# Optimization experiments

Measured on AMD Instinct MI355X. Metric: run time of the kernel, lower is better.

Reference implementation:

```python
import jax, jax.numpy as jnp
import numpy as np

B, T, D = 2, 2048, 1024
N, K, H = 16, 8, 128  # q heads, kv heads, head_dim
G = N // K            # GQA group size
EPS = 1e-6
THETA = 1000000.0
SCALE = H ** -0.5
K_MASK = float(np.finfo(np.float32).min)


def rms_norm(x, scale):
    # RMSNorm over head_dim (last axis), computed in fp32 like the original
    dtype = x.dtype
    rms = jnp.sqrt(jnp.mean(x.astype(jnp.float32) ** 2, axis=-1, keepdims=True) + EPS)
    return (scale * x / rms).astype(dtype)


def positions_from_segment_ids(seg):
    t = jnp.arange(seg.shape[1], dtype=jnp.int32)[None, :]
    off = jnp.argmax(seg, axis=1, keepdims=True).astype(jnp.int32)
    rel = t - off
    return jnp.where(seg != 0, rel, jnp.int32(2 ** 30))


def rope_sin_cos(positions):
    frac = jnp.arange(0, H, 2, dtype=jnp.float32) / H
    inv_freq = 1.0 / (THETA ** frac)                    # [H/2]
    ang = positions.astype(jnp.float32)[..., None] * inv_freq  # [B,T,H/2]
    return jnp.sin(ang), jnp.cos(ang)


def apply_rope(x, sin, cos):
    # x: [B,T,heads,H]; sin/cos: [B,T,H/2]
    x1, x2 = x[..., : H // 2], x[..., H // 2:]
    s, c = sin[:, :, None, :], cos[:, :, None, :]
    return jnp.concatenate([x1 * c - x2 * s, x2 * c + x1 * s], axis=-1).astype(x.dtype)


def setup_inputs() -> dict:
    key = jax.random.key(0)
    ks = jax.random.split(key, 8)
    std = 0.02
    return {
        "x": jax.random.normal(ks[0], (B, T, D), dtype=jnp.float32),
        "segment_ids": jnp.ones((B, T), dtype=jnp.int32),
        "wq": jax.random.normal(ks[1], (D, N, H), dtype=jnp.float32) * std,
        "wk": jax.random.normal(ks[2], (D, K, H), dtype=jnp.float32) * std,
        "wv": jax.random.normal(ks[3], (D, K, H), dtype=jnp.float32) * std,
        "wo": jax.random.normal(ks[4], (N, H, D), dtype=jnp.float32) * std,
        "q_scale": jnp.ones((H,), dtype=jnp.float32),
        "k_scale": jnp.ones((H,), dtype=jnp.float32),
    }


def reference(x, segment_ids, wq, wk, wv, wo, q_scale, k_scale):
    # QKV projections + QK RMSNorm
    q = rms_norm(jnp.einsum('BTD,DNH->BTNH', x, wq), q_scale)  # [B,T,N,H]
    k = rms_norm(jnp.einsum('BSD,DKH->BSKH', x, wk), k_scale)  # [B,T,K,H]
    v = jnp.einsum('BSD,DKH->BSKH', x, wv)                     # [B,T,K,H]

    # RoPE using segment-relative positions
    pos = positions_from_segment_ids(segment_ids)  # [B,T] int32
    sin, cos = rope_sin_cos(pos)
    q = apply_rope(q, sin, cos)
    k = apply_rope(k, sin, cos)

    # GQA attention: [B,T,K,G,H] x [B,S,K,H] -> [B,T,S,K,G]
    qg = q.reshape(B, T, K, G, H)
    logits = jnp.einsum('BTKGH,BSKH->BTSKG', qg, k) * SCALE

    causal = pos[:, None, :] <= pos[:, :, None]                       # [B,T,S]
    segm = segment_ids[:, None, :] == segment_ids[:, :, None]         # [B,T,S]
    mask = (causal & segm)[:, :, :, None, None]
    logits = jnp.where(mask, logits, K_MASK)

    w = jax.nn.softmax(logits.astype(jnp.float32), axis=2).astype(logits.dtype)
    out = jnp.einsum('BTSKG,BSKH->BTKGH', w, v).reshape(B, T, N, H)
    return jnp.einsum('BTNH,NHD->BTD', out, wo)
```

## Files before the change

### kernel.cpp

```cpp
#include <hip/hip_runtime.h>
#include <hip/hip_bf16.h>


typedef unsigned short u16;
typedef __attribute__((ext_vector_type(8))) short s16x8;
typedef __attribute__((ext_vector_type(4))) float fp32x4;
typedef __attribute__((ext_vector_type(4))) u16 u16x4;

#define MFMA_BF16(a, b, c) __builtin_amdgcn_mfma_f32_16x16x32_bf16((a), (b), (c), 0, 0, 0)

static constexpr int Bq = 2, Tq = 2048, Dq = 1024, NHq = 16, KHq = 8, Hq = 128;
static constexpr float EPSq = 1e-6f;
static constexpr float S2q = 0.08838834764831845f * 1.4426950408889634f;
static constexpr float MAXq = 20.0f;
static constexpr float NEGHUGE = -3.0e38f;

__device__ __forceinline__ u16 f2b(float f) {
  __hip_bfloat16 h = __float2bfloat16(f);
  return *reinterpret_cast<u16*>(&h);
}

__device__ __forceinline__ void gload16(const u16* g, u16* lds_base) {
  __builtin_amdgcn_global_load_lds(
      (const __attribute__((address_space(1))) unsigned int*)(const void*)g,
      (__attribute__((address_space(3))) unsigned int*)(void*)lds_base, 16, 0, 0);
}


__global__ __launch_bounds__(256) void prep_kernel(
    const float* __restrict__ x, const float* __restrict__ wq,
    const float* __restrict__ wk, const float* __restrict__ wv,
    const float* __restrict__ wo, const int* __restrict__ seg,
    u16* __restrict__ xb, u16* __restrict__ wqkv_t, u16* __restrict__ wo_t,
    int* __restrict__ pos) {
  const int bid = blockIdx.x;
  const int tid = threadIdx.x;
  if (bid < 4096) {
    const int i = bid * 1024 + tid * 4;
    const float4 v = *reinterpret_cast<const float4*>(x + i);
    u16x4 o;
    o.x = f2b(v.x); o.y = f2b(v.y); o.z = f2b(v.z); o.w = f2b(v.w);
    *reinterpret_cast<u16x4*>(xb + i) = o;
    return;
  }
  __shared__ float tile[32][33];
  __shared__ int sv[256], si[256];
  const int tx = tid & 31, ty = tid >> 5;
  if (bid < 8192) {
    const int z = bid - 4096;
    const int r0 = (z & 31) * 32;
    const int c0 = (z >> 5) * 32;
    const float* src;
    int stride, coff;
    if (c0 < 2048)      { src = wq; stride = 2048; coff = c0; }
    else if (c0 < 3072) { src = wk; stride = 1024; coff = c0 - 2048; }
    else                { src = wv; stride = 1024; coff = c0 - 3072; }
#pragma unroll
    for (int j = 0; j < 32; j += 8)
      tile[ty + j][tx] = src[(long)(r0 + ty + j) * stride + (coff + tx)];
    __syncthreads();
#pragma unroll
    for (int j = 0; j < 32; j += 8)
      wqkv_t[(long)(c0 + ty + j) * 1024 + (r0 + tx)] = f2b(tile[tx][ty + j]);
    return;
  }
  if (bid < 10240) {
    const int z = bid - 8192;
    const int c0 = (z & 31) * 32;
    const int r0 = (z >> 5) * 32;
#pragma unroll
    for (int j = 0; j < 32; j += 8)
      tile[ty + j][tx] = wo[(long)(r0 + ty + j) * 1024 + (c0 + tx)];
    __syncthreads();
#pragma unroll
    for (int j = 0; j < 32; j += 8)
      wo_t[(long)(c0 + ty + j) * 2048 + (r0 + tx)] = f2b(tile[tx][ty + j]);
    return;
  }
  const int b = bid - 10240;
  const int* s = seg + b * Tq;
  int bestv = -2147483647 - 1, besti = 0x7fffffff;
  for (int t = tid; t < Tq; t += 256) {
    int v = s[t];
    if (v > bestv) { bestv = v; besti = t; }
  }
  sv[tid] = bestv; si[tid] = besti;
  __syncthreads();
  for (int k = 128; k > 0; k >>= 1) {
    if (tid < k) {
      int v2 = sv[tid + k], i2 = si[tid + k];
      if (v2 > sv[tid] || (v2 == sv[tid] && i2 < si[tid])) {
        sv[tid] = v2; si[tid] = i2;
      }
    }
    __syncthreads();
  }
  const int off = si[0];
  for (int t = tid; t < Tq; t += 256)
    pos[b * Tq + t] = (s[t] != 0) ? (t - off) : (1 << 30);
}


__global__ __launch_bounds__(256) void gemm_qkv_kernel(
    const u16* __restrict__ A, const u16* __restrict__ Bt,
    u16* __restrict__ qkv, u16* __restrict__ vt, const int* __restrict__ pos,
    const float* __restrict__ q_scale, const float* __restrict__ k_scale) {
  __shared__ __align__(16) u16 As[128][64];
  __shared__ __align__(16) u16 Bs[128][64];
  const int tid = threadIdx.x;
  const int wave = tid >> 6, lane = tid & 63;
  const int quad = lane >> 4, l16 = lane & 15;
  const int m0 = blockIdx.y * 128, n0 = blockIdx.x * 128;
  const int row8 = lane >> 3;
  const int cgl = (lane & 7) ^ row8;

  const fp32x4 z4 = {0.f, 0.f, 0.f, 0.f};
  fp32x4 acc[2][8];
#pragma unroll
  for (int i = 0; i < 2; ++i)
#pragma unroll
    for (int j = 0; j < 8; ++j) acc[i][j] = z4;

  for (int k0 = 0; k0 < 1024; k0 += 64) {
    __syncthreads();
#pragma unroll
    for (int jj = 0; jj < 4; ++jj) {
      const int R = wave * 32 + jj * 8;
      gload16(A + (size_t)(m0 + R + row8) * 1024 + k0 + cgl * 8, &As[R][0]);
      gload16(Bt + (size_t)(n0 + R + row8) * 1024 + k0 + cgl * 8, &Bs[R][0]);
    }
    __syncthreads();
#pragma unroll
    for (int kh = 0; kh < 2; ++kh) {
      s16x8 af[2], bfr[8];
#pragma unroll
      for (int i = 0; i < 2; ++i)
        af[i] = *(const s16x8*)&As[wave * 32 + i * 16 + l16]
                               [((((kh << 2) | quad) ^ (l16 & 7)) << 3)];
#pragma unroll
      for (int j = 0; j < 8; ++j)
        bfr[j] = *(const s16x8*)&Bs[j * 16 + l16]
                                [((((kh << 2) | quad) ^ (l16 & 7)) << 3)];
#pragma unroll
      for (int i = 0; i < 2; ++i)
#pragma unroll
        for (int j = 0; j < 8; ++j) acc[i][j] = MFMA_BF16(af[i], bfr[j], acc[i][j]);
    }
  }

  const int wrow = m0 + wave * 32;
  if (n0 >= 3072) {
    const int kv8 = (n0 - 3072) >> 7;
    const int bq = wrow >> 11;
    const size_t vbase = (size_t)(bq * KHq + kv8) * Hq * Tq;
#pragma unroll
    for (int i = 0; i < 2; ++i) {
      const int t = (wrow + i * 16 + quad * 4) & 2047;
#pragma unroll
      for (int j = 0; j < 8; ++j) {
        const int h = j * 16 + l16;
        u16x4 o;
#pragma unroll
        for (int r = 0; r < 4; ++r) o[r] = f2b(acc[i][j][r]);
        *reinterpret_cast<u16x4*>(&vt[vbase + (size_t)h * Tq + t]) = o;
      }
    }
    return;
  }
  const float* scp = (n0 < 2048) ? q_scale : k_scale;
  float scl[8];
#pragma unroll
  for (int j = 0; j < 8; ++j) scl[j] = scp[j * 16 + l16];
  float invf[4];
#pragma unroll
  for (int jf = 0; jf < 4; ++jf)
    invf[jf] = __builtin_amdgcn_exp2f(
                   -(float)(jf * 16 + l16) * (19.931568569324174f / 64.0f)) *
               0.15915494309189535f;
#pragma unroll
  for (int i = 0; i < 2; ++i) {
    float ss[4] = {0.f, 0.f, 0.f, 0.f};
#pragma unroll
    for (int j = 0; j < 8; ++j)
#pragma unroll
      for (int r = 0; r < 4; ++r) ss[r] += acc[i][j][r] * acc[i][j][r];
#pragma unroll
    for (int d = 1; d < 16; d <<= 1)
#pragma unroll
      for (int r = 0; r < 4; ++r) ss[r] += __shfl_xor(ss[r], d, 64);
#pragma unroll
    for (int r = 0; r < 4; ++r) {
      const int row = wrow + i * 16 + quad * 4 + r;
      const float rinv = rsqrtf(ss[r] * (1.0f / 128.0f) + EPSq);
      const float P = (float)pos[row];
      u16* orow = qkv + (size_t)row * 4096 + n0;
#pragma unroll
      for (int jf = 0; jf < 4; ++jf) {
        float rev = P * invf[jf];
        rev -= floorf(rev);
        const float s = __builtin_amdgcn_sinf(rev);
        const float c = __builtin_amdgcn_cosf(rev);
        const float a1 = acc[i][jf][r] * rinv * scl[jf];
        const float a2 = acc[i][jf + 4][r] * rinv * scl[jf + 4];
        orow[jf * 16 + l16] = f2b(a1 * c - a2 * s);
        orow[(jf + 4) * 16 + l16] = f2b(a2 * c + a1 * s);
      }
    }
  }
}


__global__ __launch_bounds__(256) void gemm_out_kernel(
    const u16* __restrict__ A, const u16* __restrict__ Bt,
    float* __restrict__ C) {
  __shared__ __align__(16) u16 As[128][64];
  __shared__ __align__(16) u16 Bs[64][64];
  const int tid = threadIdx.x;
  const int wave = tid >> 6, lane = tid & 63;
  const int quad = lane >> 4, l16 = lane & 15;
  const int m0 = blockIdx.y * 128, n0 = blockIdx.x * 64;
  const int wm = (wave >> 1) * 64, wn = (wave & 1) * 32;
  const int row8 = lane >> 3;
  const int cgl = (lane & 7) ^ row8;

  const fp32x4 z4 = {0.f, 0.f, 0.f, 0.f};
  fp32x4 acc[4][2];
#pragma unroll
  for (int i = 0; i < 4; ++i)
#pragma unroll
    for (int j = 0; j < 2; ++j) acc[i][j] = z4;

  for (int k0 = 0; k0 < 2048; k0 += 64) {
    __syncthreads();
#pragma unroll
    for (int jj = 0; jj < 4; ++jj) {
      const int R = wave * 32 + jj * 8;
      gload16(A + (size_t)(m0 + R + row8) * 2048 + k0 + cgl * 8, &As[R][0]);
    }
#pragma unroll
    for (int jj = 0; jj < 2; ++jj) {
      const int R = wave * 16 + jj * 8;
      gload16(Bt + (size_t)(n0 + R + row8) * 2048 + k0 + cgl * 8, &Bs[R][0]);
    }
    __syncthreads();
#pragma unroll
    for (int kh = 0; kh < 2; ++kh) {
      s16x8 af[4], bfr[2];
#pragma unroll
      for (int i = 0; i < 4; ++i)
        af[i] = *(const s16x8*)&As[wm + i * 16 + l16]
                               [((((kh << 2) | quad) ^ (l16 & 7)) << 3)];
#pragma unroll
      for (int j = 0; j < 2; ++j)
        bfr[j] = *(const s16x8*)&Bs[wn + j * 16 + l16]
                                [((((kh << 2) | quad) ^ (l16 & 7)) << 3)];
#pragma unroll
      for (int i = 0; i < 4; ++i)
#pragma unroll
        for (int j = 0; j < 2; ++j) acc[i][j] = MFMA_BF16(af[i], bfr[j], acc[i][j]);
    }
  }
#pragma unroll
  for (int i = 0; i < 4; ++i) {
    const int row = m0 + wm + i * 16 + quad * 4;
#pragma unroll
    for (int j = 0; j < 2; ++j) {
      const int col = n0 + wn + j * 16 + l16;
#pragma unroll
      for (int r = 0; r < 4; ++r)
        C[(size_t)(row + r) * 1024 + col] = acc[i][j][r];
    }
  }
}


__global__ __launch_bounds__(256, 2) void flash_kernel(
    const u16* __restrict__ qkv, const u16* __restrict__ vt,
    const int* __restrict__ pos, const int* __restrict__ seg,
    u16* __restrict__ Obuf) {
  const int tid = threadIdx.x;
  const int w = tid >> 6;
  const int lane = tid & 63;
  const int quad = lane >> 4, l16 = lane & 15;
  const int qw = w >> 1;
  const int sw = w & 1;
  const int g = blockIdx.x;
  const int u = g & 31;
  const int b = u & 1;
  const int kv = (u >> 1) & 7;
  const int qh = kv * 2 + ((u >> 4) & 1);
  const int p = g >> 5;

  __shared__ __align__(16) u16 Ks[128][128];
  __shared__ __align__(16) u16 Vs[128][128];

  const u16* kbase = qkv + (size_t)(b * Tq) * 4096 + 2048 + kv * Hq;
  const u16* vbase = vt + (size_t)(b * KHq + kv) * Hq * Tq;
  const int ro = lane >> 4;
  const int ch = lane & 15;
  const fp32x4 z4 = {0.f, 0.f, 0.f, 0.f};

#pragma unroll
  for (int half = 0; half < 2; ++half) {
    const int c = half ? p : 31 - p;
    const int t0 = c * 64;
    const int nst = (c + 2) >> 1;

    s16x8 qf[2][4];
#pragma unroll
    for (int qb = 0; qb < 2; ++qb)
#pragma unroll
      for (int hk = 0; hk < 4; ++hk)
        qf[qb][hk] = *(const s16x8*)(qkv +
            (size_t)(b * Tq + t0 + qw * 32 + qb * 16 + l16) * 4096 + qh * Hq +
            hk * 32 + quad * 8);

    fp32x4 o_acc[2][8];
#pragma unroll
    for (int qb = 0; qb < 2; ++qb)
#pragma unroll
      for (int hb = 0; hb < 8; ++hb) o_acc[qb][hb] = z4;
    float l_lane[2] = {0.f, 0.f};

    for (int st = 0; st < nst; ++st) {
      const int s0 = st * 128;
      __syncthreads();
#pragma unroll
      for (int jj = 0; jj < 8; ++jj) {
        const int R = w * 32 + jj * 4;
        const int srow = R + ro;
        gload16(kbase + (size_t)(s0 + srow) * 4096 + ((ch ^ (srow & 15)) << 3),
                &Ks[R][0]);
      }
#pragma unroll
      for (int jj = 0; jj < 8; ++jj) {
        const int R = w * 32 + jj * 4;
        const int hrow = R + ro;
        gload16(vbase + (size_t)hrow * Tq + s0 + ((ch ^ (hrow & 15)) << 3),
                &Vs[R][0]);
      }
      __syncthreads();

      fp32x4 sc[2][4];
#pragma unroll
      for (int qb = 0; qb < 2; ++qb)
#pragma unroll
        for (int sh = 0; sh < 4; ++sh) sc[qb][sh] = z4;
      __builtin_amdgcn_s_setprio(1);
#pragma unroll
      for (int hk = 0; hk < 4; ++hk) {
        s16x8 kf[4];
#pragma unroll
        for (int sh = 0; sh < 4; ++sh) {
          const int srow = sw * 64 + ((sh >> 1) << 5) + ((l16 >> 2) << 3) +
                           ((sh & 1) << 2) + (l16 & 3);
          const int hc = hk * 4 + quad;
          kf[sh] = *(const s16x8*)&Ks[srow][((hc ^ (srow & 15)) << 3)];
        }
#pragma unroll
        for (int qb = 0; qb < 2; ++qb)
#pragma unroll
          for (int sh = 0; sh < 4; ++sh)
            sc[qb][sh] = MFMA_BF16(kf[sh], qf[qb][hk], sc[qb][sh]);
      }
      __builtin_amdgcn_s_setprio(0);

      if (st == nst - 1) {
        int qpos[2], qseg[2];
#pragma unroll
        for (int qb = 0; qb < 2; ++qb) {
          const int q = t0 + qw * 32 + qb * 16 + l16;
          qpos[qb] = pos[b * Tq + q];
          qseg[qb] = seg[b * Tq + q];
        }
        int spos[4][4], sseg[4][4];
#pragma unroll
        for (int sh = 0; sh < 4; ++sh)
#pragma unroll
          for (int r = 0; r < 4; ++r) {
            const int s = s0 + sw * 64 + ((sh >> 1) << 5) + quad * 8 +
                          ((sh & 1) << 2) + r;
            spos[sh][r] = pos[b * Tq + s];
            sseg[sh][r] = seg[b * Tq + s];
          }
#pragma unroll
        for (int qb = 0; qb < 2; ++qb)
#pragma unroll
          for (int sh = 0; sh < 4; ++sh)
#pragma unroll
            for (int r = 0; r < 4; ++r) {
              const bool ok = (sseg[sh][r] == qseg[qb]) &&
                              (spos[sh][r] <= qpos[qb]);
              sc[qb][sh][r] = ok ? sc[qb][sh][r] * S2q - MAXq : NEGHUGE;
            }
      } else {
#pragma unroll
        for (int qb = 0; qb < 2; ++qb)
#pragma unroll
          for (int sh = 0; sh < 4; ++sh)
#pragma unroll
            for (int r = 0; r < 4; ++r)
              sc[qb][sh][r] = sc[qb][sh][r] * S2q - MAXq;
      }

      s16x8 p8[2][2];
#pragma unroll
      for (int qb = 0; qb < 2; ++qb)
#pragma unroll
        for (int sh = 0; sh < 4; ++sh)
#pragma unroll
          for (int r = 0; r < 4; ++r) {
            const float e = __builtin_amdgcn_exp2f(sc[qb][sh][r]);
            l_lane[qb] += e;
            p8[qb][sh >> 1][(sh & 1) * 4 + r] = (short)f2b(e);
          }

      __builtin_amdgcn_s_setprio(1);
#pragma unroll
      for (int hb = 0; hb < 8; ++hb) {
        const int h = hb * 16 + l16;
        const int sch0 = sw * 8 + quad;
        const int sch1 = sw * 8 + 4 + quad;
        const s16x8 vf0 = *(const s16x8*)&Vs[h][((sch0 ^ (h & 15)) << 3)];
        const s16x8 vf1 = *(const s16x8*)&Vs[h][((sch1 ^ (h & 15)) << 3)];
#pragma unroll
        for (int qb = 0; qb < 2; ++qb) {
          o_acc[qb][hb] = MFMA_BF16(p8[qb][0], vf0, o_acc[qb][hb]);
          o_acc[qb][hb] = MFMA_BF16(p8[qb][1], vf1, o_acc[qb][hb]);
        }
      }
      __builtin_amdgcn_s_setprio(0);
    }

    __syncthreads();
    float* obuf = (float*)(&Ks[0][0]);
    float* lbuf = (float*)(&Vs[0][0]);
#pragma unroll
    for (int qb = 0; qb < 2; ++qb) {
      l_lane[qb] += __shfl_xor(l_lane[qb], 16, 64);
      l_lane[qb] += __shfl_xor(l_lane[qb], 32, 64);
    }
    if (quad == 0) {
#pragma unroll
      for (int qb = 0; qb < 2; ++qb)
        lbuf[w * 32 + qb * 16 + l16] = l_lane[qb];
    }
    if (sw == 1) {
      float* slot = obuf + qw * 4096;
#pragma unroll
      for (int qb = 0; qb < 2; ++qb)
#pragma unroll
        for (int hb = 0; hb < 8; ++hb)
          *reinterpret_cast<fp32x4*>(&slot[(qb * 8 + hb) * 256 + lane * 4]) =
              o_acc[qb][hb];
    }
    __syncthreads();
    if (sw == 0) {
      const float* slot = obuf + qw * 4096;
#pragma unroll
      for (int qb = 0; qb < 2; ++qb)
#pragma unroll
        for (int hb = 0; hb < 8; ++hb) {
          const fp32x4 t = *reinterpret_cast<const fp32x4*>(
              &slot[(qb * 8 + hb) * 256 + lane * 4]);
          o_acc[qb][hb] += t;
        }
      float inv[2][4];
#pragma unroll
      for (int qb = 0; qb < 2; ++qb)
#pragma unroll
        for (int i = 0; i < 4; ++i) {
          const int idx = qb * 16 + quad * 4 + i;
          const float lt = lbuf[(qw * 2) * 32 + idx] +
                           lbuf[(qw * 2 + 1) * 32 + idx];
          inv[qb][i] = (lt > 0.f) ? 1.f / lt : 0.f;
        }
#pragma unroll
      for (int qb = 0; qb < 2; ++qb)
#pragma unroll
        for (int hb = 0; hb < 8; ++hb)
#pragma unroll
          for (int i = 0; i < 4; ++i) {
            const int t = t0 + qw * 32 + qb * 16 + quad * 4 + i;
            Obuf[(size_t)(b * Tq + t) * 2048 + qh * Hq + hb * 16 + l16] =
                f2b(o_acc[qb][hb][i] * inv[qb][i]);
          }
    }
  }
}


extern "C" void kernel_launch(void* const* d_in, const int* in_sizes, int n_in,
                              void* d_out, int out_size, void* d_ws, size_t ws_size,
                              hipStream_t stream) {
  const float* x = (const float*)d_in[0];
  const int* seg = (const int*)d_in[1];
  const float* wq = (const float*)d_in[2];
  const float* wk = (const float*)d_in[3];
  const float* wv = (const float*)d_in[4];
  const float* wo = (const float*)d_in[5];
  const float* q_scale = (const float*)d_in[6];
  const float* k_scale = (const float*)d_in[7];
  float* out = (float*)d_out;

  char* ws = (char*)d_ws;
  u16* xb = (u16*)(ws);
  u16* wqkv_t = (u16*)(ws + 8388608);
  u16* qkv = (u16*)(ws + 16777216);
  u16* vt = (u16*)(ws + 50331648);
  u16* wo_t = (u16*)(ws + 58720256);
  u16* Obuf = (u16*)(ws + 62914560);
  int* posb = (int*)(ws + 79691776);

  prep_kernel<<<10242, 256, 0, stream>>>(x, wq, wk, wv, wo, seg,
                                         xb, wqkv_t, wo_t, posb);

  gemm_qkv_kernel<<<dim3(32, 32, 1), 256, 0, stream>>>(
      xb, wqkv_t, qkv, vt, posb, q_scale, k_scale);

  flash_kernel<<<512, 256, 0, stream>>>(qkv, vt, posb, seg, Obuf);

  gemm_out_kernel<<<dim3(16, 32, 1), 256, 0, stream>>>(Obuf, wo_t, out);
}
```

Baseline: 225.4 us.

## Split flash attention key tile across four waves with 512-thread blocks

Doubles the flash kernel block to 512 threads so each 128-key tile is split across four waves per query group instead of two, halving per-wave score and PV work per tile. Each wave loads half as many K/V rows. Split barriers with vmcnt waits let QK^T start once K has landed while V is still loading. The epilogue gains an extra cross-wave reduction stage through LDS and four-way row-sum combination, adding synchronization and LDS traffic in exchange for more waves in flight per CU.

```diff
diff --git a/kernel.cpp b/kernel.cpp
--- a/kernel.cpp
+++ b/kernel.cpp
@@ -274,7 +274,7 @@
 }
 
 
-__global__ __launch_bounds__(256, 2) void flash_kernel(
+__global__ __launch_bounds__(512, 4) void flash_kernel(
     const u16* __restrict__ qkv, const u16* __restrict__ vt,
     const int* __restrict__ pos, const int* __restrict__ seg,
     u16* __restrict__ Obuf) {
@@ -282,8 +282,8 @@
   const int w = tid >> 6;
   const int lane = tid & 63;
   const int quad = lane >> 4, l16 = lane & 15;
-  const int qw = w >> 1;
-  const int sw = w & 1;
+  const int qw = w >> 2;
+  const int sw = w & 3;
   const int g = blockIdx.x;
   const int u = g & 31;
   const int b = u & 1;
@@ -291,8 +291,10 @@
   const int qh = kv * 2 + ((u >> 4) & 1);
   const int p = g >> 5;
 
-  __shared__ __align__(16) u16 Ks[128][128];
-  __shared__ __align__(16) u16 Vs[128][128];
+  __shared__ __align__(16) u16 smem[2 * 128 * 128];
+  __shared__ float lbuf[256];
+  u16* ksp = smem;
+  u16* vsp = smem + 128 * 128;
 
   const u16* kbase = qkv + (size_t)(b * Tq) * 4096 + 2048 + kv * Hq;
   const u16* vbase = vt + (size_t)(b * KHq + kv) * Hq * Tq;
@@ -326,42 +328,41 @@
       const int s0 = st * 128;
       __syncthreads();
 #pragma unroll
-      for (int jj = 0; jj < 8; ++jj) {
-        const int R = w * 32 + jj * 4;
+      for (int j = 0; j < 4; ++j) {
+        const int R = w * 16 + j * 4;
         const int srow = R + ro;
         gload16(kbase + (size_t)(s0 + srow) * 4096 + ((ch ^ (srow & 15)) << 3),
-                &Ks[R][0]);
-      }
-#pragma unroll
-      for (int jj = 0; jj < 8; ++jj) {
-        const int R = w * 32 + jj * 4;
+                ksp + R * 128);
+      }
+#pragma unroll
+      for (int j = 0; j < 4; ++j) {
+        const int R = w * 16 + j * 4;
         const int hrow = R + ro;
         gload16(vbase + (size_t)hrow * Tq + s0 + ((ch ^ (hrow & 15)) << 3),
-                &Vs[R][0]);
-      }
-      __syncthreads();
-
-      fp32x4 sc[2][4];
-#pragma unroll
-      for (int qb = 0; qb < 2; ++qb)
-#pragma unroll
-        for (int sh = 0; sh < 4; ++sh) sc[qb][sh] = z4;
+                vsp + R * 128);
+      }
+      asm volatile("s_waitcnt vmcnt(4)" ::: "memory");
+      __builtin_amdgcn_s_barrier();
+      __builtin_amdgcn_sched_barrier(0);
+
+      fp32x4 sc[2][2];
+#pragma unroll
+      for (int qb = 0; qb < 2; ++qb) { sc[qb][0] = z4; sc[qb][1] = z4; }
       __builtin_amdgcn_s_setprio(1);
 #pragma unroll
       for (int hk = 0; hk < 4; ++hk) {
-        s16x8 kf[4];
-#pragma unroll
-        for (int sh = 0; sh < 4; ++sh) {
-          const int srow = sw * 64 + ((sh >> 1) << 5) + ((l16 >> 2) << 3) +
-                           ((sh & 1) << 2) + (l16 & 3);
+        s16x8 kf[2];
+#pragma unroll
+        for (int sh = 0; sh < 2; ++sh) {
+          const int srow = sw * 32 + ((l16 >> 2) << 3) + (sh << 2) + (l16 & 3);
           const int hc = hk * 4 + quad;
-          kf[sh] = *(const s16x8*)&Ks[srow][((hc ^ (srow & 15)) << 3)];
+          kf[sh] = *(const s16x8*)&ksp[srow * 128 + ((hc ^ (srow & 15)) << 3)];
         }
 #pragma unroll
-        for (int qb = 0; qb < 2; ++qb)
-#pragma unroll
-          for (int sh = 0; sh < 4; ++sh)
-            sc[qb][sh] = MFMA_BF16(kf[sh], qf[qb][hk], sc[qb][sh]);
+        for (int qb = 0; qb < 2; ++qb) {
+          sc[qb][0] = MFMA_BF16(kf[0], qf[qb][hk], sc[qb][0]);
+          sc[qb][1] = MFMA_BF16(kf[1], qf[qb][hk], sc[qb][1]);
+        }
       }
       __builtin_amdgcn_s_setprio(0);
 
@@ -373,20 +374,19 @@
           qpos[qb] = pos[b * Tq + q];
           qseg[qb] = seg[b * Tq + q];
         }
-        int spos[4][4], sseg[4][4];
-#pragma unroll
-        for (int sh = 0; sh < 4; ++sh)
+        int spos[2][4], sseg[2][4];
+#pragma unroll
+        for (int sh = 0; sh < 2; ++sh)
 #pragma unroll
           for (int r = 0; r < 4; ++r) {
-            const int s = s0 + sw * 64 + ((sh >> 1) << 5) + quad * 8 +
-                          ((sh & 1) << 2) + r;
+            const int s = s0 + sw * 32 + quad * 8 + sh * 4 + r;
             spos[sh][r] = pos[b * Tq + s];
             sseg[sh][r] = seg[b * Tq + s];
           }
 #pragma unroll
         for (int qb = 0; qb < 2; ++qb)
 #pragma unroll
-          for (int sh = 0; sh < 4; ++sh)
+          for (int sh = 0; sh < 2; ++sh)
 #pragma unroll
             for (int r = 0; r < 4; ++r) {
               const bool ok = (sseg[sh][r] == qseg[qb]) &&
@@ -397,44 +397,43 @@
 #pragma unroll
         for (int qb = 0; qb < 2; ++qb)
 #pragma unroll
-          for (int sh = 0; sh < 4; ++sh)
+          for (int sh = 0; sh < 2; ++sh)
 #pragma unroll
             for (int r = 0; r < 4; ++r)
               sc[qb][sh][r] = sc[qb][sh][r] * S2q - MAXq;
       }
 
-      s16x8 p8[2][2];
-#pragma unroll
-      for (int qb = 0; qb < 2; ++qb)
-#pragma unroll
-        for (int sh = 0; sh < 4; ++sh)
+      s16x8 p8[2];
+#pragma unroll
+      for (int qb = 0; qb < 2; ++qb)
+#pragma unroll
+        for (int sh = 0; sh < 2; ++sh)
 #pragma unroll
           for (int r = 0; r < 4; ++r) {
             const float e = __builtin_amdgcn_exp2f(sc[qb][sh][r]);
             l_lane[qb] += e;
-            p8[qb][sh >> 1][(sh & 1) * 4 + r] = (short)f2b(e);
+            p8[qb][sh * 4 + r] = (short)f2b(e);
           }
+
+      asm volatile("s_waitcnt vmcnt(0)" ::: "memory");
+      __builtin_amdgcn_s_barrier();
+      __builtin_amdgcn_sched_barrier(0);
 
       __builtin_amdgcn_s_setprio(1);
 #pragma unroll
       for (int hb = 0; hb < 8; ++hb) {
         const int h = hb * 16 + l16;
-        const int sch0 = sw * 8 + quad;
-        const int sch1 = sw * 8 + 4 + quad;
-        const s16x8 vf0 = *(const s16x8*)&Vs[h][((sch0 ^ (h & 15)) << 3)];
-        const s16x8 vf1 = *(const s16x8*)&Vs[h][((sch1 ^ (h & 15)) << 3)];
-#pragma unroll
-        for (int qb = 0; qb < 2; ++qb) {
-          o_acc[qb][hb] = MFMA_BF16(p8[qb][0], vf0, o_acc[qb][hb]);
-          o_acc[qb][hb] = MFMA_BF16(p8[qb][1], vf1, o_acc[qb][hb]);
-        }
+        const int sch = sw * 4 + quad;
+        const s16x8 vf = *(const s16x8*)&vsp[h * 128 + ((sch ^ (h & 15)) << 3)];
+#pragma unroll
+        for (int qb = 0; qb < 2; ++qb)
+          o_acc[qb][hb] = MFMA_BF16(p8[qb], vf, o_acc[qb][hb]);
       }
       __builtin_amdgcn_s_setprio(0);
     }
 
     __syncthreads();
-    float* obuf = (float*)(&Ks[0][0]);
-    float* lbuf = (float*)(&Vs[0][0]);
+    float* obuf = (float*)smem;
 #pragma unroll
     for (int qb = 0; qb < 2; ++qb) {
       l_lane[qb] += __shfl_xor(l_lane[qb], 16, 64);
@@ -443,10 +442,10 @@
     if (quad == 0) {
 #pragma unroll
       for (int qb = 0; qb < 2; ++qb)
-        lbuf[w * 32 + qb * 16 + l16] = l_lane[qb];
-    }
-    if (sw == 1) {
-      float* slot = obuf + qw * 4096;
+        lbuf[sw * 64 + qw * 32 + qb * 16 + l16] = l_lane[qb];
+    }
+    if (sw >= 2) {
+      float* slot = obuf + (qw * 2 + (sw - 2)) * 4096;
 #pragma unroll
       for (int qb = 0; qb < 2; ++qb)
 #pragma unroll
@@ -455,8 +454,28 @@
               o_acc[qb][hb];
     }
     __syncthreads();
+    if (sw < 2) {
+      float* slot = obuf + (qw * 2 + sw) * 4096;
+#pragma unroll
+      for (int qb = 0; qb < 2; ++qb)
+#pragma unroll
+        for (int hb = 0; hb < 8; ++hb) {
+          const fp32x4 t = *reinterpret_cast<const fp32x4*>(
+              &slot[(qb * 8 + hb) * 256 + lane * 4]);
+          o_acc[qb][hb] += t;
+        }
+      if (sw == 1) {
+#pragma unroll
+        for (int qb = 0; qb < 2; ++qb)
+#pragma unroll
+          for (int hb = 0; hb < 8; ++hb)
+            *reinterpret_cast<fp32x4*>(&slot[(qb * 8 + hb) * 256 + lane * 4]) =
+                o_acc[qb][hb];
+      }
+    }
+    __syncthreads();
     if (sw == 0) {
-      const float* slot = obuf + qw * 4096;
+      const float* slot = obuf + (qw * 2 + 1) * 4096;
 #pragma unroll
       for (int qb = 0; qb < 2; ++qb)
 #pragma unroll
@@ -470,9 +489,9 @@
       for (int qb = 0; qb < 2; ++qb)
 #pragma unroll
         for (int i = 0; i < 4; ++i) {
-          const int idx = qb * 16 + quad * 4 + i;
-          const float lt = lbuf[(qw * 2) * 32 + idx] +
-                           lbuf[(qw * 2 + 1) * 32 + idx];
+          const int qq = qw * 32 + qb * 16 + quad * 4 + i;
+          const float lt = lbuf[qq] + lbuf[64 + qq] + lbuf[128 + qq] +
+                           lbuf[192 + qq];
           inv[qb][i] = (lt > 0.f) ? 1.f / lt : 0.f;
         }
 #pragma unroll
@@ -518,7 +537,7 @@
   gemm_qkv_kernel<<<dim3(32, 32, 1), 256, 0, stream>>>(
       xb, wqkv_t, qkv, vt, posb, q_scale, k_scale);
 
-  flash_kernel<<<512, 256, 0, stream>>>(qkv, vt, posb, seg, Obuf);
+  flash_kernel<<<512, 512, 0, stream>>>(qkv, vt, posb, seg, Obuf);
 
   gemm_out_kernel<<<dim3(16, 32, 1), 256, 0, stream>>>(Obuf, wo_t, out);
 }
```

Measured after the change: 336.8 us. +49.4%, slower.
